# Performance work log

Measured on AMD Instinct MI355X. Metric: run time of the kernel, lower is better.

## Reference

```python
import jax, jax.numpy as jnp
import numpy as np

D = 512
H = 8
G = 4          # GroupNorm groups
EPS = 1e-3     # GroupNorm eps


def group_norm(x):
    # x: (b, n, t, d); torch code normalizes per (batch, group) over (n*t, d/G)
    b, n, t, d = x.shape
    xr = x.reshape(b, n * t, G, d // G)
    mu = xr.mean(axis=(1, 3), keepdims=True)
    var = ((xr - mu) ** 2).mean(axis=(1, 3), keepdims=True)
    return ((xr - mu) * jax.lax.rsqrt(var + EPS)).reshape(b, n, t, d)


def setup_inputs() -> dict:
    key = jax.random.key(0)
    ks = jax.random.split(key, 9)
    s = 1.0 / np.sqrt(D)
    inp = {
        "ind": 0,
        "in_f": jax.random.normal(ks[0], (4, 8, 512, D), dtype=jnp.float32),
        "in_f_kv": jax.random.normal(ks[1], (4, 8, 512, D), dtype=jnp.float32),
        "Wq": jax.random.normal(ks[2], (D, D), dtype=jnp.float32) * s,
        "Wk": jax.random.normal(ks[3], (D, D), dtype=jnp.float32) * s,
        "Wv": jax.random.normal(ks[4], (D, D), dtype=jnp.float32) * s,
        "Wz": jax.random.normal(ks[5], (D, D), dtype=jnp.float32) * s,
        "bz": jnp.zeros((D,), dtype=jnp.float32),
        "W1": jax.random.normal(ks[6], (D, D), dtype=jnp.float32) * s,
        "b1": jnp.full((D,), 0.1, dtype=jnp.float32),
        "W2": jax.random.normal(ks[7], (D, D), dtype=jnp.float32) * s,
        "b2": jnp.full((D,), 0.1, dtype=jnp.float32),
    }
    return inp


def reference(ind, in_f, in_f_kv, Wq, Wk, Wv, Wz, bz, W1, b1, W2, b2):
    b, n, t, d = in_f.shape
    hd = d // H
    scale = 1.0 / np.sqrt(hd)

    _in_f = group_norm(in_f)          # LN_1
    _in_f_kv = group_norm(in_f_kv)    # LN_2

    # torch Linear: y = x @ W.T
    q = group_norm(_in_f @ Wq.T)      # LN_3
    k = group_norm(_in_f_kv @ Wk.T)   # LN_4
    v = _in_f_kv @ Wv.T

    q = q.reshape(b, n, t, H, hd)
    k = k.reshape(b, n, -1, H, hd)
    v = v.reshape(b, n, -1, H, hd)

    logits = jnp.einsum('bnqhd,bnkhd->bnhqk', q, k) * scale
    attn_weights = jax.nn.softmax(logits, axis=-1)
    attn_out = jnp.einsum('bnhqk,bnkhd->bnqhd', attn_weights, v).reshape(b, n, t, d)

    in_f_u1 = attn_out @ Wz.T + bz
    in_f_u2 = jax.nn.leaky_relu(_in_f @ W1.T + b1, negative_slope=0.01) @ W2.T + b2

    out_f = in_f + in_f_u1 + in_f_u2
    return (out_f, attn_weights)
```

## Files before the change

kernel.cpp:

```cpp
#include <hip/hip_runtime.h>
#include <math.h>

#define TDIM 512
#define DDIM 512
#define NTROWS 4096
#define MROWS 16384
#define EPSGN 1e-3f

typedef __attribute__((ext_vector_type(8))) short bf16x8;
typedef __attribute__((ext_vector_type(4))) float f32x4;
typedef __attribute__((ext_vector_type(8))) unsigned short us8;
typedef __attribute__((ext_vector_type(4))) unsigned short us4;

__device__ __forceinline__ unsigned short f2b(float f) {
  unsigned int u = __float_as_uint(f);
  return (unsigned short)((u + 0x7fffu + ((u >> 16) & 1u)) >> 16);
}
__device__ __forceinline__ float b2f(unsigned short h) {
  return __uint_as_float(((unsigned int)h) << 16);
}

#define GLOAD16(g, l)                                                                   \
  __builtin_amdgcn_global_load_lds((const __attribute__((address_space(1))) void*)(g),  \
                                   (__attribute__((address_space(3))) void*)(l), 16, 0, 0)

__global__ __launch_bounds__(256) void gn_stats_w(const float* __restrict__ x0,
                                                  const float* __restrict__ x1,
                                                  float* __restrict__ p0,
                                                  float* __restrict__ p1,
                                                  const float* w0, const float* w1,
                                                  const float* w2, const float* w3,
                                                  const float* w4, const float* w5,
                                                  unsigned short* __restrict__ wdst) {
  if (blockIdx.z == 2) {
    const int bid = blockIdx.x + (blockIdx.y << 4);
    for (int c = bid * 256 + threadIdx.x; c < 196608; c += 512 * 256) {
      const int t = c >> 15;
      const int off = c & 32767;
      const float* s;
      switch (t) {
        case 0: s = w0; break; case 1: s = w1; break; case 2: s = w2; break;
        case 3: s = w3; break; case 4: s = w4; break; default: s = w5; break;
      }
      const float4 f0 = *(const float4*)(s + (size_t)off * 8);
      const float4 f1 = *(const float4*)(s + (size_t)off * 8 + 4);
      us8 o;
      o[0] = f2b(f0.x); o[1] = f2b(f0.y); o[2] = f2b(f0.z); o[3] = f2b(f0.w);
      o[4] = f2b(f1.x); o[5] = f2b(f1.y); o[6] = f2b(f1.z); o[7] = f2b(f1.w);
      *(us8*)(wdst + (size_t)c * 8) = o;
    }
    return;
  }
  const float* x = blockIdx.z ? x1 : x0;
  float* part = blockIdx.z ? p1 : p0;
  const int grp = blockIdx.x;
  const int chunk = blockIdx.y;
  const int b = grp >> 2, g = grp & 3;
  const float* base = x + (size_t)b * NTROWS * DDIM + g * 128;
  const int r0 = chunk * (NTROWS / 32);
  float s = 0.f, sq = 0.f;
  for (int i = threadIdx.x; i < 128 * 32; i += 256) {
    const int r = i >> 5, c4 = (i & 31) << 2;
    const float4 v = *(const float4*)(base + (size_t)(r0 + r) * DDIM + c4);
    s += v.x + v.y + v.z + v.w;
    sq += v.x * v.x + v.y * v.y + v.z * v.z + v.w * v.w;
  }
#pragma unroll
  for (int o = 32; o > 0; o >>= 1) { s += __shfl_down(s, o); sq += __shfl_down(sq, o); }
  __shared__ float red[8];
  const int wid = threadIdx.x >> 6;
  if ((threadIdx.x & 63) == 0) { red[wid * 2] = s; red[wid * 2 + 1] = sq; }
  __syncthreads();
  if (threadIdx.x == 0) {
    float S = 0.f, SQ = 0.f;
    for (int w = 0; w < 4; ++w) { S += red[w * 2]; SQ += red[w * 2 + 1]; }
    part[(grp * 32 + chunk) * 2] = S;
    part[(grp * 32 + chunk) * 2 + 1] = SQ;
  }
}

__global__ __launch_bounds__(256) void cvt_gn(const float* __restrict__ x0,
                                              const float* __restrict__ x1,
                                              const float* __restrict__ p0,
                                              const float* __restrict__ p1,
                                              unsigned short* __restrict__ o0,
                                              unsigned short* __restrict__ o1) {
  const float* x = blockIdx.y ? x1 : x0;
  const float* part = blockIdx.y ? p1 : p0;
  unsigned short* o = blockIdx.y ? o1 : o0;
  __shared__ float sstat[32];
  if (threadIdx.x < 16) {
    const float* p = part + threadIdx.x * 64;
    float S = 0.f, SQ = 0.f;
    for (int c = 0; c < 32; ++c) { S += p[c * 2]; SQ += p[c * 2 + 1]; }
    const float inv = 1.f / (float)(NTROWS * 128);
    const float mu = S * inv;
    const float var = SQ * inv - mu * mu;
    sstat[threadIdx.x * 2] = mu;
    sstat[threadIdx.x * 2 + 1] = rsqrtf(var + EPSGN);
  }
  __syncthreads();
  const int NC = MROWS * DDIM / 8;
  for (int c = blockIdx.x * 256 + threadIdx.x; c < NC; c += gridDim.x * 256) {
    const int e = c * 8;
    const int row = e >> 9;
    const int ch = e & 511;
    const int sidx = (((row >> 12) << 2) | (ch >> 7)) << 1;
    const float mu = sstat[sidx], rs = sstat[sidx + 1];
    const float4 f0 = *(const float4*)(x + (size_t)e);
    const float4 f1 = *(const float4*)(x + (size_t)e + 4);
    us8 v;
    v[0] = f2b((f0.x - mu) * rs); v[1] = f2b((f0.y - mu) * rs);
    v[2] = f2b((f0.z - mu) * rs); v[3] = f2b((f0.w - mu) * rs);
    v[4] = f2b((f1.x - mu) * rs); v[5] = f2b((f1.y - mu) * rs);
    v[6] = f2b((f1.z - mu) * rs); v[7] = f2b((f1.w - mu) * rs);
    *(us8*)(o + (size_t)e) = v;
  }
}

__global__ __launch_bounds__(256) void gemm_all(const unsigned short* __restrict__ a16,
                                                const unsigned short* __restrict__ akv16,
                                                const unsigned short* __restrict__ w16,
                                                unsigned short* __restrict__ q16,
                                                unsigned short* __restrict__ h16,
                                                unsigned short* __restrict__ k16,
                                                unsigned short* __restrict__ vTb,
                                                const float* __restrict__ b1,
                                                float* __restrict__ part_q,
                                                float* __restrict__ part_k,
                                                float* __restrict__ sk) {
  __shared__ __align__(16) unsigned short As[128 * 64];
  __shared__ __align__(16) unsigned short Bs[128 * 64];
  __shared__ float red[8];
  const int tid = threadIdx.x;
  const int wave = tid >> 6, lane = tid & 63;
  const int bm = blockIdx.x << 7;
  const int z = blockIdx.z;
  const bool first = blockIdx.y < 4;
  const unsigned short* A = z ? akv16 : a16;
  const unsigned short* B = w16 + (size_t)262144 * (z ? (first ? 1 : 2) : (first ? 0 : 4));
  const int bnl = (blockIdx.y & 3) << 7;
  const int wr = (wave >> 1) << 6;
  const int wc = (wave & 1) << 6;
  const int lr = lane & 15, lg = lane >> 4;

  f32x4 acc[4][4] = {};
  const int srow = lane >> 3;
  const int sslot = (lane & 7) ^ srow;

  for (int k0 = 0; k0 < 512; k0 += 64) {
    __syncthreads();
#pragma unroll
    for (int i = 0; i < 4; ++i) {
      const int ci = wave * 4 + i;
      const int row = ci * 8 + srow;
      GLOAD16(A + (size_t)(bm + row) * 512 + k0 + sslot * 8, (char*)As + ci * 1024);
      GLOAD16(B + (size_t)(bnl + row) * 512 + k0 + sslot * 8, (char*)Bs + ci * 1024);
    }
    __syncthreads();
#pragma unroll
    for (int kk = 0; kk < 64; kk += 32) {
      bf16x8 af[4], bfr[4];
#pragma unroll
      for (int i = 0; i < 4; ++i) {
        const int row = wr + i * 16 + lr;
        af[i] = *(const bf16x8*)&As[row * 64 + ((((kk >> 3) + lg) ^ (row & 7)) << 3)];
      }
#pragma unroll
      for (int j = 0; j < 4; ++j) {
        const int row = wc + j * 16 + lr;
        bfr[j] = *(const bf16x8*)&Bs[row * 64 + ((((kk >> 3) + lg) ^ (row & 7)) << 3)];
      }
#pragma unroll
      for (int i = 0; i < 4; ++i)
#pragma unroll
        for (int j = 0; j < 4; ++j)
          acc[i][j] = __builtin_amdgcn_mfma_f32_16x16x32_bf16(af[i], bfr[j], acc[i][j], 0, 0, 0);
    }
  }

  if (first) {
    unsigned short* C0 = z ? k16 : q16;
#pragma unroll
    for (int i = 0; i < 4; ++i) {
      const int row0 = bm + wr + i * 16 + lg * 4;
#pragma unroll
      for (int j = 0; j < 4; ++j) {
        const int col = bnl + wc + j * 16 + lr;
#pragma unroll
        for (int r = 0; r < 4; ++r)
          C0[(size_t)(row0 + r) * 512 + col] = f2b(acc[i][j][r]);
      }
    }
    float s = 0.f, sq = 0.f;
#pragma unroll
    for (int i = 0; i < 4; ++i)
#pragma unroll
      for (int j = 0; j < 4; ++j)
#pragma unroll
        for (int r = 0; r < 4; ++r) { const float v = acc[i][j][r]; s += v; sq += v * v; }
#pragma unroll
    for (int o = 32; o > 0; o >>= 1) { s += __shfl_xor(s, o); sq += __shfl_xor(sq, o); }
    if (lane == 0) { red[wave * 2] = s; red[wave * 2 + 1] = sq; }
    __syncthreads();
    if (tid == 0) {
      float* part = z ? part_k : part_q;
      const float S = red[0] + red[2] + red[4] + red[6];
      const float SQ = red[1] + red[3] + red[5] + red[7];
      const int batch = blockIdx.x >> 5, slot = blockIdx.x & 31, g = blockIdx.y;
      const int idx = ((((batch << 2) | g) << 5) | slot) << 1;
      part[idx] = S;
      part[idx + 1] = SQ;
    }
    if (z) {
      const int head = (bnl >> 6) + (wave & 1);
#pragma unroll
      for (int i = 0; i < 4; ++i) {
#pragma unroll
        for (int r = 0; r < 4; ++r) {
          float t = acc[i][0][r] + acc[i][1][r] + acc[i][2][r] + acc[i][3][r];
#pragma unroll
          for (int o = 1; o < 16; o <<= 1) t += __shfl_xor(t, o);
          if (lr == 0)
            sk[(size_t)(bm + wr + i * 16 + lg * 4 + r) * 8 + head] = t;
        }
      }
    }
  } else if (z == 0) {
#pragma unroll
    for (int i = 0; i < 4; ++i) {
      const int row0 = bm + wr + i * 16 + lg * 4;
#pragma unroll
      for (int j = 0; j < 4; ++j) {
        const int col = bnl + wc + j * 16 + lr;
        const float bb = b1[col];
#pragma unroll
        for (int r = 0; r < 4; ++r) {
          float v = acc[i][j][r] + bb;
          v = v > 0.f ? v : 0.01f * v;
          h16[(size_t)(row0 + r) * 512 + col] = f2b(v);
        }
      }
    }
  } else {
#pragma unroll
    for (int i = 0; i < 4; ++i) {
      const int row0 = bm + wr + i * 16 + lg * 4;
#pragma unroll
      for (int j = 0; j < 4; ++j) {
        const int col = bnl + wc + j * 16 + lr;
        us4 pk;
#pragma unroll
        for (int r = 0; r < 4; ++r) pk[r] = f2b(acc[i][j][r]);
        *(us4*)&vTb[((size_t)(row0 >> 9) * 512 + col) * 512 + (row0 & 511)] = pk;
      }
    }
  }
}

__global__ __launch_bounds__(256) void gemm_final(const unsigned short* __restrict__ A0,
                                                  const unsigned short* __restrict__ A1,
                                                  const unsigned short* __restrict__ B0,
                                                  const unsigned short* __restrict__ B1,
                                                  float* __restrict__ Cf,
                                                  const float* __restrict__ bias0,
                                                  const float* __restrict__ bias1,
                                                  const float* __restrict__ init) {
  __shared__ __align__(16) unsigned short As[128 * 64];
  __shared__ __align__(16) unsigned short Bs[128 * 64];
  const int tid = threadIdx.x;
  const int wave = tid >> 6, lane = tid & 63;
  const int bm = blockIdx.x << 7, bn = blockIdx.y << 7;
  const int wr = (wave >> 1) << 6;
  const int wc = (wave & 1) << 6;
  const int lr = lane & 15, lg = lane >> 4;

  f32x4 acc[4][4] = {};
  const int srow = lane >> 3;
  const int sslot = (lane & 7) ^ srow;

  for (int k0 = 0; k0 < 1024; k0 += 64) {
    const unsigned short* Ab = (k0 < 512) ? A0 : A1;
    const unsigned short* Bb = (k0 < 512) ? B0 : B1;
    const int kl = k0 & 511;
    __syncthreads();
#pragma unroll
    for (int i = 0; i < 4; ++i) {
      const int ci = wave * 4 + i;
      const int row = ci * 8 + srow;
      GLOAD16(Ab + (size_t)(bm + row) * 512 + kl + sslot * 8, (char*)As + ci * 1024);
      GLOAD16(Bb + (size_t)(bn + row) * 512 + kl + sslot * 8, (char*)Bs + ci * 1024);
    }
    __syncthreads();
#pragma unroll
    for (int kk = 0; kk < 64; kk += 32) {
      bf16x8 af[4], bfr[4];
#pragma unroll
      for (int i = 0; i < 4; ++i) {
        const int row = wr + i * 16 + lr;
        af[i] = *(const bf16x8*)&As[row * 64 + ((((kk >> 3) + lg) ^ (row & 7)) << 3)];
      }
#pragma unroll
      for (int j = 0; j < 4; ++j) {
        const int row = wc + j * 16 + lr;
        bfr[j] = *(const bf16x8*)&Bs[row * 64 + ((((kk >> 3) + lg) ^ (row & 7)) << 3)];
      }
#pragma unroll
      for (int i = 0; i < 4; ++i)
#pragma unroll
        for (int j = 0; j < 4; ++j)
          acc[i][j] = __builtin_amdgcn_mfma_f32_16x16x32_bf16(af[i], bfr[j], acc[i][j], 0, 0, 0);
    }
  }

#pragma unroll
  for (int i = 0; i < 4; ++i) {
    const int row0 = bm + wr + i * 16 + lg * 4;
#pragma unroll
    for (int j = 0; j < 4; ++j) {
      const int col = bn + wc + j * 16 + lr;
      const float bb = bias0[col] + bias1[col];
#pragma unroll
      for (int r = 0; r < 4; ++r) {
        const size_t o = (size_t)(row0 + r) * 512 + col;
        Cf[o] = acc[i][j][r] + bb + init[o];
      }
    }
  }
}

__global__ __launch_bounds__(256) void attn_fused(const unsigned short* __restrict__ q16,
                                                  const unsigned short* __restrict__ k16,
                                                  const unsigned short* __restrict__ vT,
                                                  const float* __restrict__ part_q,
                                                  const float* __restrict__ part_k,
                                                  const float* __restrict__ sk,
                                                  float* __restrict__ aw,
                                                  unsigned short* __restrict__ ao16) {
  __shared__ __align__(16) unsigned short Qs[64 * 64];
  __shared__ __align__(16) unsigned short Ks[256 * 64];
  __shared__ __align__(16) unsigned short Ps[64 * 256];
  __shared__ float WM[4][64];
  __shared__ float WS[4][64];
  __shared__ float sk_lds[512];
  __shared__ float cst[2];

  const int bid = blockIdx.x;
  const int q0 = blockIdx.y << 6;
  const int h = bid & 7;
  const int b = bid >> 6;
  const int tid = threadIdx.x;
  const int w = tid >> 6, lane = tid & 63;
  const int lr = lane & 15, lg = lane >> 4;
  const int srow = lane >> 3;
  const int sslot = (lane & 7) ^ srow;

  const size_t hb = (size_t)(bid >> 3) * (512 * 512);
  const unsigned short* Qg = q16 + hb + h * 64;
  const unsigned short* Kg = k16 + hb + h * 64;
  const unsigned short* Vg = vT + hb + (size_t)h * 64 * 512;

  if (tid == 0) {
    const int pbase = (((b << 2) | (h >> 1)) << 6);
    const float* pq = part_q + pbase;
    const float* pk = part_k + pbase;
    float Sq = 0.f, SQq = 0.f, Sk = 0.f, SQk = 0.f;
    for (int c = 0; c < 32; ++c) {
      Sq += pq[c * 2]; SQq += pq[c * 2 + 1];
      Sk += pk[c * 2]; SQk += pk[c * 2 + 1];
    }
    const float inv = 1.f / (float)(NTROWS * 128);
    const float muq = Sq * inv, vq = SQq * inv - muq * muq;
    const float muk = Sk * inv, vk = SQk * inv - muk * muk;
    const float a = rsqrtf(vq + EPSGN) * rsqrtf(vk + EPSGN) * 0.125f;
    cst[0] = a;
    cst[1] = a * muq;
  }
  {
    const float* skg = sk + (size_t)(bid >> 3) * 512 * 8 + h;
    for (int j = tid; j < 512; j += 256) sk_lds[j] = skg[(size_t)j * 8];
  }

#pragma unroll
  for (int it = 0; it < 2; ++it) {
    const int ci = w * 2 + it;
    const int row = ci * 8 + srow;
    GLOAD16(Qg + (size_t)(q0 + row) * 512 + sslot * 8, (char*)Qs + ci * 1024);
  }

  f32x4 sc[4][8] = {};

#pragma unroll
  for (int half = 0; half < 2; ++half) {
    __syncthreads();
#pragma unroll
    for (int it = 0; it < 8; ++it) {
      const int ci = w * 8 + it;
      const int row = ci * 8 + srow;
      GLOAD16(Kg + (size_t)(half * 256 + row) * 512 + sslot * 8, (char*)Ks + ci * 1024);
    }
    __syncthreads();
#pragma unroll
    for (int kk = 0; kk < 64; kk += 32) {
      bf16x8 aq[4];
#pragma unroll
      for (int qf = 0; qf < 4; ++qf) {
        const int row = qf * 16 + lr;
        aq[qf] = *(const bf16x8*)&Qs[row * 64 + ((((kk >> 3) + lg) ^ (row & 7)) << 3)];
      }
#pragma unroll
      for (int kf = 0; kf < 4; ++kf) {
        const int row = w * 64 + kf * 16 + lr;
        const bf16x8 bk = *(const bf16x8*)&Ks[row * 64 + ((((kk >> 3) + lg) ^ (row & 7)) << 3)];
#pragma unroll
        for (int qf = 0; qf < 4; ++qf)
          sc[qf][half * 4 + kf] =
              __builtin_amdgcn_mfma_f32_16x16x32_bf16(aq[qf], bk, sc[qf][half * 4 + kf], 0, 0, 0);
      }
    }
  }

  const float aSc = cst[0], cmu = cst[1];
#pragma unroll
  for (int qf = 0; qf < 4; ++qf)
#pragma unroll
    for (int kfi = 0; kfi < 8; ++kfi) {
      const int k = ((kfi >> 2) << 8) + w * 64 + ((kfi & 3) << 4) + lr;
      const float corr = cmu * sk_lds[k];
#pragma unroll
      for (int r = 0; r < 4; ++r) sc[qf][kfi][r] = aSc * sc[qf][kfi][r] - corr;
    }

  float Mv[4][4];
#pragma unroll
  for (int qf = 0; qf < 4; ++qf)
#pragma unroll
    for (int r = 0; r < 4; ++r) {
      float m = sc[qf][0][r];
#pragma unroll
      for (int kf = 1; kf < 8; ++kf) m = fmaxf(m, sc[qf][kf][r]);
#pragma unroll
      for (int o = 1; o < 16; o <<= 1) m = fmaxf(m, __shfl_xor(m, o));
      Mv[qf][r] = m;
    }
  if (lr == 0) {
#pragma unroll
    for (int qf = 0; qf < 4; ++qf)
#pragma unroll
      for (int r = 0; r < 4; ++r) WM[w][qf * 16 + lg * 4 + r] = Mv[qf][r];
  }
  __syncthreads();
#pragma unroll
  for (int qf = 0; qf < 4; ++qf)
#pragma unroll
    for (int r = 0; r < 4; ++r) {
      const int q = qf * 16 + lg * 4 + r;
      Mv[qf][r] = fmaxf(fmaxf(WM[0][q], WM[1][q]), fmaxf(WM[2][q], WM[3][q]));
    }
  float sl[4][4] = {};
#pragma unroll
  for (int qf = 0; qf < 4; ++qf)
#pragma unroll
    for (int kf = 0; kf < 8; ++kf) {
      f32x4 v = sc[qf][kf];
#pragma unroll
      for (int r = 0; r < 4; ++r) {
        const float e = __expf(v[r] - Mv[qf][r]);
        v[r] = e;
        sl[qf][r] += e;
      }
      sc[qf][kf] = v;
    }
#pragma unroll
  for (int qf = 0; qf < 4; ++qf)
#pragma unroll
    for (int r = 0; r < 4; ++r) {
      float s = sl[qf][r];
#pragma unroll
      for (int o = 1; o < 16; o <<= 1) s += __shfl_xor(s, o);
      sl[qf][r] = s;
    }
  if (lr == 0) {
#pragma unroll
    for (int qf = 0; qf < 4; ++qf)
#pragma unroll
      for (int r = 0; r < 4; ++r) WS[w][qf * 16 + lg * 4 + r] = sl[qf][r];
  }
  __syncthreads();
#pragma unroll
  for (int qf = 0; qf < 4; ++qf)
#pragma unroll
    for (int r = 0; r < 4; ++r) {
      const int q = qf * 16 + lg * 4 + r;
      const float inv = 1.f / (WS[0][q] + WS[1][q] + WS[2][q] + WS[3][q]);
#pragma unroll
      for (int kf = 0; kf < 8; ++kf) sc[qf][kf][r] *= inv;
    }

  float* AWp = aw + ((size_t)bid * 512 + q0) * 512;
#pragma unroll
  for (int qf = 0; qf < 4; ++qf)
#pragma unroll
    for (int kfi = 0; kfi < 8; ++kfi) {
      const int k = ((kfi >> 2) << 8) + w * 64 + ((kfi & 3) << 4) + lr;
#pragma unroll
      for (int r = 0; r < 4; ++r)
        __builtin_nontemporal_store(sc[qf][kfi][r],
                                    &AWp[(size_t)(qf * 16 + lg * 4 + r) * 512 + k]);
    }

  f32x4 accO[4] = {};
#pragma unroll
  for (int half = 0; half < 2; ++half) {
    __syncthreads();
#pragma unroll
    for (int it = 0; it < 8; ++it) {
      const int ci = w * 8 + it;
      const int row = ci * 2 + (lane >> 5);
      const int s = lane & 31;
      GLOAD16(Vg + (size_t)row * 512 + half * 256 + ((s ^ (row & 7)) << 3),
              (char*)Ks + ci * 1024);
    }
#pragma unroll
    for (int qf = 0; qf < 4; ++qf)
#pragma unroll
      for (int r = 0; r < 4; ++r) {
        const int q = qf * 16 + lg * 4 + r;
#pragma unroll
        for (int kf = 0; kf < 4; ++kf) {
          const int k = w * 64 + (kf << 4) + lr;
          Ps[q * 256 + (((k >> 3) ^ (q & 7)) << 3) + (k & 7)] = f2b(sc[qf][half * 4 + kf][r]);
        }
      }
    __syncthreads();
#pragma unroll
    for (int ks = 0; ks < 256; ks += 32) {
      const int sl0 = ks >> 3;
      const int q = w * 16 + lr;
      const bf16x8 af = *(const bf16x8*)&Ps[q * 256 + (((sl0 + lg) ^ (q & 7)) << 3)];
#pragma unroll
      for (int df = 0; df < 4; ++df) {
        const int row = df * 16 + lr;
        const bf16x8 vb = *(const bf16x8*)&Ks[row * 256 + (((sl0 + lg) ^ (row & 7)) << 3)];
        accO[df] = __builtin_amdgcn_mfma_f32_16x16x32_bf16(af, vb, accO[df], 0, 0, 0);
      }
    }
  }

  const int growb = (bid >> 3) * 512 + q0 + w * 16 + lg * 4;
#pragma unroll
  for (int df = 0; df < 4; ++df)
#pragma unroll
    for (int r = 0; r < 4; ++r)
      ao16[(size_t)(growb + r) * 512 + h * 64 + df * 16 + lr] = f2b(accO[df][r]);
}

extern "C" void kernel_launch(void* const* d_in, const int* in_sizes, int n_in,
                              void* d_out, int out_size, void* d_ws, size_t ws_size,
                              hipStream_t stream) {
  const float* in_f = (const float*)d_in[1];
  const float* in_fkv = (const float*)d_in[2];
  const float* Wq = (const float*)d_in[3];
  const float* Wk = (const float*)d_in[4];
  const float* Wv = (const float*)d_in[5];
  const float* Wz = (const float*)d_in[6];
  const float* bz = (const float*)d_in[7];
  const float* W1 = (const float*)d_in[8];
  const float* b1 = (const float*)d_in[9];
  const float* W2 = (const float*)d_in[10];
  const float* b2 = (const float*)d_in[11];

  float* out_f = (float*)d_out;
  float* attw = out_f + (size_t)MROWS * DDIM;

  const size_t TSB = (size_t)MROWS * DDIM;
  unsigned short* us = (unsigned short*)d_ws;
  unsigned short* a16 = us;
  unsigned short* akv16 = us + TSB;
  unsigned short* q16 = us + 2 * TSB;
  unsigned short* k16 = us + 3 * TSB;
  unsigned short* h16 = us + 4 * TSB;
  unsigned short* ao16 = us + 5 * TSB;
  unsigned short* vT = us + 6 * TSB;
  unsigned short* w16 = us + 7 * TSB;
  float* fbase = (float*)(us + 7 * TSB + 6 * 262144);
  float* part0 = fbase;
  float* part1 = fbase + 1024;
  float* part_q = fbase + 2048;
  float* part_k = fbase + 3072;
  float* sk = fbase + 4096;

  gn_stats_w<<<dim3(16, 32, 3), 256, 0, stream>>>(in_f, in_fkv, part0, part1, Wq, Wk, Wv, Wz,
                                                  W1, W2, w16);
  cvt_gn<<<dim3(2048, 2), 256, 0, stream>>>(in_f, in_fkv, part0, part1, a16, akv16);
  gemm_all<<<dim3(128, 8, 2), 256, 0, stream>>>(a16, akv16, w16, q16, h16, k16, vT, b1, part_q,
                                                part_k, sk);
  attn_fused<<<dim3(256, 8), 256, 0, stream>>>(q16, k16, vT, part_q, part_k, sk, attw, ao16);
  gemm_final<<<dim3(128, 4), 256, 0, stream>>>(ao16, h16, w16 + 3 * 262144, w16 + 5 * 262144,
                                               out_f, bz, b2, in_f);
}
```

Measured before the change: 247.5 us.

## Double-buffer K and V tiles in 128-row chunks in attention kernel

The attention kernel now splits the K and V staging into four 128-row chunks held in two LDS buffers. The next chunk is loaded asynchronously while MFMAs run on the current one, so QK^T and PV no longer stall on a full 256-row load. The first V chunk is issued before the softmax so it overlaps with that work, and P is written to LDS per chunk in a double buffer as well. LDS footprint stays about the same, but there are more barriers and more complex indexing.

```diff
diff --git a/kernel.cpp b/kernel.cpp
--- a/kernel.cpp
+++ b/kernel.cpp
@@ -338,8 +338,8 @@
                                                   float* __restrict__ aw,
                                                   unsigned short* __restrict__ ao16) {
   __shared__ __align__(16) unsigned short Qs[64 * 64];
-  __shared__ __align__(16) unsigned short Ks[256 * 64];
-  __shared__ __align__(16) unsigned short Ps[64 * 256];
+  __shared__ __align__(16) unsigned short Kbuf[2][128 * 64];
+  __shared__ __align__(16) unsigned short Pbuf[2][64 * 128];
   __shared__ float WM[4][64];
   __shared__ float WS[4][64];
   __shared__ float sk_lds[512];
@@ -387,19 +387,28 @@
     const int row = ci * 8 + srow;
     GLOAD16(Qg + (size_t)(q0 + row) * 512 + sslot * 8, (char*)Qs + ci * 1024);
   }
+#pragma unroll
+  for (int i = 0; i < 4; ++i) {
+    const int ci = w * 4 + i;
+    const int row = ci * 8 + srow;
+    GLOAD16(Kg + (size_t)row * 512 + sslot * 8, (char*)&Kbuf[0][0] + ci * 1024);
+  }
+  __syncthreads();
 
   f32x4 sc[4][8] = {};
-
-#pragma unroll
-  for (int half = 0; half < 2; ++half) {
-    __syncthreads();
-#pragma unroll
-    for (int it = 0; it < 8; ++it) {
-      const int ci = w * 8 + it;
-      const int row = ci * 8 + srow;
-      GLOAD16(Kg + (size_t)(half * 256 + row) * 512 + sslot * 8, (char*)Ks + ci * 1024);
-    }
-    __syncthreads();
+  int cur = 0;
+#pragma unroll
+  for (int qr = 0; qr < 4; ++qr) {
+    if (qr < 3) {
+      const int nb = cur ^ 1;
+#pragma unroll
+      for (int i = 0; i < 4; ++i) {
+        const int ci = w * 4 + i;
+        const int row = ci * 8 + srow;
+        GLOAD16(Kg + (size_t)((qr + 1) * 128 + row) * 512 + sslot * 8,
+                (char*)&Kbuf[nb][0] + ci * 1024);
+      }
+    }
 #pragma unroll
     for (int kk = 0; kk < 64; kk += 32) {
       bf16x8 aq[4];
@@ -409,26 +418,37 @@
         aq[qf] = *(const bf16x8*)&Qs[row * 64 + ((((kk >> 3) + lg) ^ (row & 7)) << 3)];
       }
 #pragma unroll
-      for (int kf = 0; kf < 4; ++kf) {
-        const int row = w * 64 + kf * 16 + lr;
-        const bf16x8 bk = *(const bf16x8*)&Ks[row * 64 + ((((kk >> 3) + lg) ^ (row & 7)) << 3)];
+      for (int kfq = 0; kfq < 2; ++kfq) {
+        const int rl = w * 32 + kfq * 16 + lr;
+        const bf16x8 bk =
+            *(const bf16x8*)&Kbuf[cur][rl * 64 + ((((kk >> 3) + lg) ^ (rl & 7)) << 3)];
 #pragma unroll
         for (int qf = 0; qf < 4; ++qf)
-          sc[qf][half * 4 + kf] =
-              __builtin_amdgcn_mfma_f32_16x16x32_bf16(aq[qf], bk, sc[qf][half * 4 + kf], 0, 0, 0);
-      }
-    }
+          sc[qf][qr * 2 + kfq] =
+              __builtin_amdgcn_mfma_f32_16x16x32_bf16(aq[qf], bk, sc[qf][qr * 2 + kfq], 0, 0, 0);
+      }
+    }
+    __syncthreads();
+    cur ^= 1;
+  }
+
+#pragma unroll
+  for (int i = 0; i < 4; ++i) {
+    const int ci = w * 4 + i;
+    const int vd = ci * 4 + (lane >> 4);
+    const int vs = ((lane & 15) ^ (vd & 7)) << 3;
+    GLOAD16(Vg + (size_t)vd * 512 + vs, (char*)&Kbuf[0][0] + ci * 1024);
   }
 
   const float aSc = cst[0], cmu = cst[1];
 #pragma unroll
   for (int qf = 0; qf < 4; ++qf)
 #pragma unroll
-    for (int kfi = 0; kfi < 8; ++kfi) {
-      const int k = ((kfi >> 2) << 8) + w * 64 + ((kfi & 3) << 4) + lr;
+    for (int s = 0; s < 8; ++s) {
+      const int k = ((s >> 1) << 7) + w * 32 + ((s & 1) << 4) + lr;
       const float corr = cmu * sk_lds[k];
 #pragma unroll
-      for (int r = 0; r < 4; ++r) sc[qf][kfi][r] = aSc * sc[qf][kfi][r] - corr;
+      for (int r = 0; r < 4; ++r) sc[qf][s][r] = aSc * sc[qf][s][r] - corr;
     }
 
   float Mv[4][4];
@@ -497,54 +517,73 @@
       for (int kf = 0; kf < 8; ++kf) sc[qf][kf][r] *= inv;
     }
 
+#pragma unroll
+  for (int qf = 0; qf < 4; ++qf)
+#pragma unroll
+    for (int r = 0; r < 4; ++r) {
+      const int q = qf * 16 + lg * 4 + r;
+#pragma unroll
+      for (int kfq = 0; kfq < 2; ++kfq) {
+        const int kl = w * 32 + kfq * 16 + lr;
+        Pbuf[0][q * 128 + (((kl >> 3) ^ (q & 7)) << 3) + (kl & 7)] = f2b(sc[qf][kfq][r]);
+      }
+    }
+
   float* AWp = aw + ((size_t)bid * 512 + q0) * 512;
 #pragma unroll
   for (int qf = 0; qf < 4; ++qf)
 #pragma unroll
-    for (int kfi = 0; kfi < 8; ++kfi) {
-      const int k = ((kfi >> 2) << 8) + w * 64 + ((kfi & 3) << 4) + lr;
+    for (int s = 0; s < 8; ++s) {
+      const int k = ((s >> 1) << 7) + w * 32 + ((s & 1) << 4) + lr;
 #pragma unroll
       for (int r = 0; r < 4; ++r)
-        __builtin_nontemporal_store(sc[qf][kfi][r],
+        __builtin_nontemporal_store(sc[qf][s][r],
                                     &AWp[(size_t)(qf * 16 + lg * 4 + r) * 512 + k]);
     }
+  __syncthreads();
 
   f32x4 accO[4] = {};
-#pragma unroll
-  for (int half = 0; half < 2; ++half) {
+  cur = 0;
+#pragma unroll
+  for (int qr = 0; qr < 4; ++qr) {
+    if (qr < 3) {
+      const int nb = cur ^ 1;
+#pragma unroll
+      for (int i = 0; i < 4; ++i) {
+        const int ci = w * 4 + i;
+        const int vd = ci * 4 + (lane >> 4);
+        const int vs = ((lane & 15) ^ (vd & 7)) << 3;
+        GLOAD16(Vg + (size_t)vd * 512 + (qr + 1) * 128 + vs,
+                (char*)&Kbuf[nb][0] + ci * 1024);
+      }
+#pragma unroll
+      for (int qf = 0; qf < 4; ++qf)
+#pragma unroll
+        for (int r = 0; r < 4; ++r) {
+          const int q = qf * 16 + lg * 4 + r;
+#pragma unroll
+          for (int kfq = 0; kfq < 2; ++kfq) {
+            const int kl = w * 32 + kfq * 16 + lr;
+            Pbuf[nb][q * 128 + (((kl >> 3) ^ (q & 7)) << 3) + (kl & 7)] =
+                f2b(sc[qf][(qr + 1) * 2 + kfq][r]);
+          }
+        }
+    }
+#pragma unroll
+    for (int ks = 0; ks < 128; ks += 32) {
+      const int q = w * 16 + lr;
+      const bf16x8 af =
+          *(const bf16x8*)&Pbuf[cur][q * 128 + ((((ks >> 3) + lg) ^ (q & 7)) << 3)];
+#pragma unroll
+      for (int df = 0; df < 4; ++df) {
+        const int vrow = df * 16 + lr;
+        const bf16x8 vb =
+            *(const bf16x8*)&Kbuf[cur][vrow * 128 + ((((ks >> 3) + lg) ^ (vrow & 7)) << 3)];
+        accO[df] = __builtin_amdgcn_mfma_f32_16x16x32_bf16(af, vb, accO[df], 0, 0, 0);
+      }
+    }
     __syncthreads();
-#pragma unroll
-    for (int it = 0; it < 8; ++it) {
-      const int ci = w * 8 + it;
-      const int row = ci * 2 + (lane >> 5);
-      const int s = lane & 31;
-      GLOAD16(Vg + (size_t)row * 512 + half * 256 + ((s ^ (row & 7)) << 3),
-              (char*)Ks + ci * 1024);
-    }
-#pragma unroll
-    for (int qf = 0; qf < 4; ++qf)
-#pragma unroll
-      for (int r = 0; r < 4; ++r) {
-        const int q = qf * 16 + lg * 4 + r;
-#pragma unroll
-        for (int kf = 0; kf < 4; ++kf) {
-          const int k = w * 64 + (kf << 4) + lr;
-          Ps[q * 256 + (((k >> 3) ^ (q & 7)) << 3) + (k & 7)] = f2b(sc[qf][half * 4 + kf][r]);
-        }
-      }
-    __syncthreads();
-#pragma unroll
-    for (int ks = 0; ks < 256; ks += 32) {
-      const int sl0 = ks >> 3;
-      const int q = w * 16 + lr;
-      const bf16x8 af = *(const bf16x8*)&Ps[q * 256 + (((sl0 + lg) ^ (q & 7)) << 3)];
-#pragma unroll
-      for (int df = 0; df < 4; ++df) {
-        const int row = df * 16 + lr;
-        const bf16x8 vb = *(const bf16x8*)&Ks[row * 256 + (((sl0 + lg) ^ (row & 7)) << 3)];
-        accO[df] = __builtin_amdgcn_mfma_f32_16x16x32_bf16(af, vb, accO[df], 0, 0, 0);
-      }
-    }
+    cur ^= 1;
   }
 
   const int growb = (bid >> 3) * 512 + q0 + w * 16 + lg * 4;
```

Result: slower. 252.7 us (+2.1%).

## Fold input GroupNorm into per-batch weights and fuse stats with bf16 conversion

Applied to the files above, without the earlier changes.

Computes GroupNorm statistics in the same pass that converts the raw fp32 inputs to bf16, so the inputs are read once instead of twice. The normalization is then applied algebraically: each projection weight is scaled per batch by the group rsqrt, and a per-output-column mean correction term is subtracted in the GEMM epilogue. The final GEMM also reads the residual from the bf16 copy of the input rather than the fp32 original, which halves that traffic. In exchange it adds per-batch weight copies and a small weight-prep kernel, and it loses precision in the residual add and in the mean subtraction.

```diff
diff --git a/kernel.cpp b/kernel.cpp
--- a/kernel.cpp
+++ b/kernel.cpp
@@ -24,103 +24,110 @@
   __builtin_amdgcn_global_load_lds((const __attribute__((address_space(1))) void*)(g),  \
                                    (__attribute__((address_space(3))) void*)(l), 16, 0, 0)
 
-__global__ __launch_bounds__(256) void gn_stats_w(const float* __restrict__ x0,
-                                                  const float* __restrict__ x1,
-                                                  float* __restrict__ p0,
-                                                  float* __restrict__ p1,
-                                                  const float* w0, const float* w1,
-                                                  const float* w2, const float* w3,
-                                                  const float* w4, const float* w5,
-                                                  unsigned short* __restrict__ wdst) {
-  if (blockIdx.z == 2) {
-    const int bid = blockIdx.x + (blockIdx.y << 4);
-    for (int c = bid * 256 + threadIdx.x; c < 196608; c += 512 * 256) {
-      const int t = c >> 15;
-      const int off = c & 32767;
-      const float* s;
-      switch (t) {
-        case 0: s = w0; break; case 1: s = w1; break; case 2: s = w2; break;
-        case 3: s = w3; break; case 4: s = w4; break; default: s = w5; break;
-      }
-      const float4 f0 = *(const float4*)(s + (size_t)off * 8);
-      const float4 f1 = *(const float4*)(s + (size_t)off * 8 + 4);
-      us8 o;
-      o[0] = f2b(f0.x); o[1] = f2b(f0.y); o[2] = f2b(f0.z); o[3] = f2b(f0.w);
-      o[4] = f2b(f1.x); o[5] = f2b(f1.y); o[6] = f2b(f1.z); o[7] = f2b(f1.w);
-      *(us8*)(wdst + (size_t)c * 8) = o;
-    }
+__global__ __launch_bounds__(256) void stats_cvt(const float* __restrict__ x0,
+                                                 const float* __restrict__ x1,
+                                                 unsigned short* __restrict__ o0,
+                                                 unsigned short* __restrict__ o1,
+                                                 float* __restrict__ p0,
+                                                 float* __restrict__ p1) {
+  const float* x = blockIdx.y ? x1 : x0;
+  unsigned short* o = blockIdx.y ? o1 : o0;
+  float* part = blockIdx.y ? p1 : p0;
+  const int blk = blockIdx.x;
+  const int batch = blk >> 6;
+  const int chunk = blk & 63;
+  const size_t base = (size_t)blk * 64 * 512;
+  const int tid = threadIdx.x;
+  float s = 0.f, sq = 0.f;
+#pragma unroll 4
+  for (int it = 0; it < 16; ++it) {
+    const size_t e = base + (size_t)it * 2048 + (size_t)tid * 8;
+    const float4 f0 = *(const float4*)(x + e);
+    const float4 f1 = *(const float4*)(x + e + 4);
+    us8 v;
+    v[0] = f2b(f0.x); v[1] = f2b(f0.y); v[2] = f2b(f0.z); v[3] = f2b(f0.w);
+    v[4] = f2b(f1.x); v[5] = f2b(f1.y); v[6] = f2b(f1.z); v[7] = f2b(f1.w);
+    *(us8*)(o + e) = v;
+    s += f0.x + f0.y + f0.z + f0.w + f1.x + f1.y + f1.z + f1.w;
+    sq += f0.x * f0.x + f0.y * f0.y + f0.z * f0.z + f0.w * f0.w +
+          f1.x * f1.x + f1.y * f1.y + f1.z * f1.z + f1.w * f1.w;
+  }
+  const int wave = tid >> 6, lane = tid & 63;
+#pragma unroll
+  for (int of = 1; of < 16; of <<= 1) { s += __shfl_xor(s, of); sq += __shfl_xor(sq, of); }
+  __shared__ float red[4][4][2];
+  if ((lane & 15) == 0) { red[wave][lane >> 4][0] = s; red[wave][lane >> 4][1] = sq; }
+  __syncthreads();
+  if (tid < 4) {
+    float S = 0.f, SQ = 0.f;
+#pragma unroll
+    for (int w = 0; w < 4; ++w) { S += red[w][tid][0]; SQ += red[w][tid][1]; }
+    const int idx = (((batch << 2) | tid) << 6) | chunk;
+    part[idx * 2] = S;
+    part[idx * 2 + 1] = SQ;
+  }
+}
+
+__global__ __launch_bounds__(256) void wprep(const float* __restrict__ Wq,
+                                             const float* __restrict__ Wk,
+                                             const float* __restrict__ Wv,
+                                             const float* __restrict__ W1,
+                                             const float* __restrict__ Wz,
+                                             const float* __restrict__ W2,
+                                             const float* __restrict__ p0,
+                                             const float* __restrict__ p1,
+                                             unsigned short* __restrict__ w16s,
+                                             float* __restrict__ corr) {
+  const int y = blockIdx.y;
+  if (y >= 16) {
+    const float* s = (y == 16) ? Wz : W2;
+    unsigned short* d = w16s + (size_t)y * 262144;
+    const int c = blockIdx.x * 256 + threadIdx.x;
+    const float4 f0 = *(const float4*)(s + (size_t)c * 8);
+    const float4 f1 = *(const float4*)(s + (size_t)c * 8 + 4);
+    us8 v;
+    v[0] = f2b(f0.x); v[1] = f2b(f0.y); v[2] = f2b(f0.z); v[3] = f2b(f0.w);
+    v[4] = f2b(f1.x); v[5] = f2b(f1.y); v[6] = f2b(f1.z); v[7] = f2b(f1.w);
+    *(us8*)(d + (size_t)c * 8) = v;
     return;
   }
-  const float* x = blockIdx.z ? x1 : x0;
-  float* part = blockIdx.z ? p1 : p0;
-  const int grp = blockIdx.x;
-  const int chunk = blockIdx.y;
-  const int b = grp >> 2, g = grp & 3;
-  const float* base = x + (size_t)b * NTROWS * DDIM + g * 128;
-  const int r0 = chunk * (NTROWS / 32);
-  float s = 0.f, sq = 0.f;
-  for (int i = threadIdx.x; i < 128 * 32; i += 256) {
-    const int r = i >> 5, c4 = (i & 31) << 2;
-    const float4 v = *(const float4*)(base + (size_t)(r0 + r) * DDIM + c4);
-    s += v.x + v.y + v.z + v.w;
-    sq += v.x * v.x + v.y * v.y + v.z * v.z + v.w * v.w;
-  }
-#pragma unroll
-  for (int o = 32; o > 0; o >>= 1) { s += __shfl_down(s, o); sq += __shfl_down(sq, o); }
-  __shared__ float red[8];
-  const int wid = threadIdx.x >> 6;
-  if ((threadIdx.x & 63) == 0) { red[wid * 2] = s; red[wid * 2 + 1] = sq; }
-  __syncthreads();
-  if (threadIdx.x == 0) {
+  const int w = y >> 2, b = y & 3;
+  const float* W = (w == 0) ? Wq : (w == 1) ? Wk : (w == 2) ? Wv : W1;
+  const float* part = (w == 0 || w == 3) ? p0 : p1;
+  __shared__ float mrs[4][2];
+  if (threadIdx.x < 4) {
+    const float* p = part + (((b << 2) | threadIdx.x) << 6) * 2;
     float S = 0.f, SQ = 0.f;
-    for (int w = 0; w < 4; ++w) { S += red[w * 2]; SQ += red[w * 2 + 1]; }
-    part[(grp * 32 + chunk) * 2] = S;
-    part[(grp * 32 + chunk) * 2 + 1] = SQ;
-  }
-}
-
-__global__ __launch_bounds__(256) void cvt_gn(const float* __restrict__ x0,
-                                              const float* __restrict__ x1,
-                                              const float* __restrict__ p0,
-                                              const float* __restrict__ p1,
-                                              unsigned short* __restrict__ o0,
-                                              unsigned short* __restrict__ o1) {
-  const float* x = blockIdx.y ? x1 : x0;
-  const float* part = blockIdx.y ? p1 : p0;
-  unsigned short* o = blockIdx.y ? o1 : o0;
-  __shared__ float sstat[32];
-  if (threadIdx.x < 16) {
-    const float* p = part + threadIdx.x * 64;
-    float S = 0.f, SQ = 0.f;
-    for (int c = 0; c < 32; ++c) { S += p[c * 2]; SQ += p[c * 2 + 1]; }
+    for (int c = 0; c < 64; ++c) { S += p[c * 2]; SQ += p[c * 2 + 1]; }
     const float inv = 1.f / (float)(NTROWS * 128);
     const float mu = S * inv;
     const float var = SQ * inv - mu * mu;
-    sstat[threadIdx.x * 2] = mu;
-    sstat[threadIdx.x * 2 + 1] = rsqrtf(var + EPSGN);
+    const float rs = rsqrtf(var + EPSGN);
+    mrs[threadIdx.x][0] = rs;
+    mrs[threadIdx.x][1] = mu * rs;
   }
   __syncthreads();
-  const int NC = MROWS * DDIM / 8;
-  for (int c = blockIdx.x * 256 + threadIdx.x; c < NC; c += gridDim.x * 256) {
-    const int e = c * 8;
-    const int row = e >> 9;
-    const int ch = e & 511;
-    const int sidx = (((row >> 12) << 2) | (ch >> 7)) << 1;
-    const float mu = sstat[sidx], rs = sstat[sidx + 1];
-    const float4 f0 = *(const float4*)(x + (size_t)e);
-    const float4 f1 = *(const float4*)(x + (size_t)e + 4);
-    us8 v;
-    v[0] = f2b((f0.x - mu) * rs); v[1] = f2b((f0.y - mu) * rs);
-    v[2] = f2b((f0.z - mu) * rs); v[3] = f2b((f0.w - mu) * rs);
-    v[4] = f2b((f1.x - mu) * rs); v[5] = f2b((f1.y - mu) * rs);
-    v[6] = f2b((f1.z - mu) * rs); v[7] = f2b((f1.w - mu) * rs);
-    *(us8*)(o + (size_t)e) = v;
-  }
+  const int wave = threadIdx.x >> 6, lane = threadIdx.x & 63;
+  const int n = blockIdx.x * 4 + wave;
+  const int k = lane * 8;
+  const int g = lane >> 4;
+  const float rs = mrs[g][0], murs = mrs[g][1];
+  const float4 f0 = *(const float4*)(W + (size_t)n * 512 + k);
+  const float4 f1 = *(const float4*)(W + (size_t)n * 512 + k + 4);
+  us8 v;
+  v[0] = f2b(f0.x * rs); v[1] = f2b(f0.y * rs); v[2] = f2b(f0.z * rs); v[3] = f2b(f0.w * rs);
+  v[4] = f2b(f1.x * rs); v[5] = f2b(f1.y * rs); v[6] = f2b(f1.z * rs); v[7] = f2b(f1.w * rs);
+  *(us8*)(w16s + (size_t)((w << 2) | b) * 262144 + (size_t)n * 512 + k) = v;
+  float t = (f0.x + f0.y + f0.z + f0.w + f1.x + f1.y + f1.z + f1.w) * murs;
+#pragma unroll
+  for (int of = 1; of < 64; of <<= 1) t += __shfl_xor(t, of);
+  if (lane == 0) corr[(((w << 2) | b) << 9) | n] = t;
 }
 
 __global__ __launch_bounds__(256) void gemm_all(const unsigned short* __restrict__ a16,
                                                 const unsigned short* __restrict__ akv16,
-                                                const unsigned short* __restrict__ w16,
+                                                const unsigned short* __restrict__ w16s,
+                                                const float* __restrict__ corr,
                                                 unsigned short* __restrict__ q16,
                                                 unsigned short* __restrict__ h16,
                                                 unsigned short* __restrict__ k16,
@@ -135,10 +142,12 @@
   const int tid = threadIdx.x;
   const int wave = tid >> 6, lane = tid & 63;
   const int bm = blockIdx.x << 7;
+  const int batch = blockIdx.x >> 5;
   const int z = blockIdx.z;
   const bool first = blockIdx.y < 4;
+  const int widx = z ? (first ? 1 : 2) : (first ? 0 : 3);
   const unsigned short* A = z ? akv16 : a16;
-  const unsigned short* B = w16 + (size_t)262144 * (z ? (first ? 1 : 2) : (first ? 0 : 4));
+  const unsigned short* B = w16s + (size_t)262144 * ((widx << 2) | batch);
   const int bnl = (blockIdx.y & 3) << 7;
   const int wr = (wave >> 1) << 6;
   const int wc = (wave & 1) << 6;
@@ -179,6 +188,19 @@
     }
   }
 
+  {
+    const float* cb = corr + (((widx << 2) | batch) << 9);
+    float cj[4];
+#pragma unroll
+    for (int j = 0; j < 4; ++j) cj[j] = cb[bnl + wc + j * 16 + lr];
+#pragma unroll
+    for (int i = 0; i < 4; ++i)
+#pragma unroll
+      for (int j = 0; j < 4; ++j)
+#pragma unroll
+        for (int r = 0; r < 4; ++r) acc[i][j][r] -= cj[j];
+  }
+
   if (first) {
     unsigned short* C0 = z ? k16 : q16;
 #pragma unroll
@@ -207,7 +229,7 @@
       float* part = z ? part_k : part_q;
       const float S = red[0] + red[2] + red[4] + red[6];
       const float SQ = red[1] + red[3] + red[5] + red[7];
-      const int batch = blockIdx.x >> 5, slot = blockIdx.x & 31, g = blockIdx.y;
+      const int slot = blockIdx.x & 31, g = blockIdx.y;
       const int idx = ((((batch << 2) | g) << 5) | slot) << 1;
       part[idx] = S;
       part[idx + 1] = SQ;
@@ -265,7 +287,7 @@
                                                   float* __restrict__ Cf,
                                                   const float* __restrict__ bias0,
                                                   const float* __restrict__ bias1,
-                                                  const float* __restrict__ init) {
+                                                  const unsigned short* __restrict__ init16) {
   __shared__ __align__(16) unsigned short As[128 * 64];
   __shared__ __align__(16) unsigned short Bs[128 * 64];
   const int tid = threadIdx.x;
@@ -323,7 +345,7 @@
 #pragma unroll
       for (int r = 0; r < 4; ++r) {
         const size_t o = (size_t)(row0 + r) * 512 + col;
-        Cf[o] = acc[i][j][r] + bb + init[o];
+        Cf[o] = acc[i][j][r] + bb + b2f(init16[o]);
       }
     }
   }
@@ -582,20 +604,20 @@
   unsigned short* h16 = us + 4 * TSB;
   unsigned short* ao16 = us + 5 * TSB;
   unsigned short* vT = us + 6 * TSB;
-  unsigned short* w16 = us + 7 * TSB;
-  float* fbase = (float*)(us + 7 * TSB + 6 * 262144);
-  float* part0 = fbase;
-  float* part1 = fbase + 1024;
-  float* part_q = fbase + 2048;
-  float* part_k = fbase + 3072;
-  float* sk = fbase + 4096;
-
-  gn_stats_w<<<dim3(16, 32, 3), 256, 0, stream>>>(in_f, in_fkv, part0, part1, Wq, Wk, Wv, Wz,
-                                                  W1, W2, w16);
-  cvt_gn<<<dim3(2048, 2), 256, 0, stream>>>(in_f, in_fkv, part0, part1, a16, akv16);
-  gemm_all<<<dim3(128, 8, 2), 256, 0, stream>>>(a16, akv16, w16, q16, h16, k16, vT, b1, part_q,
-                                                part_k, sk);
+  unsigned short* w16s = us + 7 * TSB;
+  float* fbase = (float*)(us + 7 * TSB + 18 * 262144);
+  float* p0 = fbase;
+  float* p1 = fbase + 2048;
+  float* part_q = fbase + 4096;
+  float* part_k = fbase + 5120;
+  float* corr = fbase + 6144;
+  float* sk = fbase + 14336;
+
+  stats_cvt<<<dim3(256, 2), 256, 0, stream>>>(in_f, in_fkv, a16, akv16, p0, p1);
+  wprep<<<dim3(128, 18), 256, 0, stream>>>(Wq, Wk, Wv, W1, Wz, W2, p0, p1, w16s, corr);
+  gemm_all<<<dim3(128, 8, 2), 256, 0, stream>>>(a16, akv16, w16s, corr, q16, h16, k16, vT, b1,
+                                                part_q, part_k, sk);
   attn_fused<<<dim3(256, 8), 256, 0, stream>>>(q16, k16, vT, part_q, part_k, sk, attw, ao16);
-  gemm_final<<<dim3(128, 4), 256, 0, stream>>>(ao16, h16, w16 + 3 * 262144, w16 + 5 * 262144,
-                                               out_f, bz, b2, in_f);
-}
+  gemm_final<<<dim3(128, 4), 256, 0, stream>>>(ao16, h16, w16s + 16 * 262144,
+                                               w16s + 17 * 262144, out_f, bz, b2, a16);
+}
```

Measured after the change: 241.1 us. 2.6% less time.
